# Kernel tuning notes

Hardware: AMD Instinct MI355X
Metric: run time of the kernel (lower is better)

Reference implementation:

```python
import math
import jax, jax.numpy as jnp
import numpy as np
from jax import lax

G_RATIO = 0.5       # g_ratio init arg
TMAX_RATIO = 0.25


def setup_inputs() -> dict:
    key = jax.random.key(0)
    k1, k2, k3, k4 = jax.random.split(key, 4)
    N = 4096
    cost_maps = jax.random.uniform(k1, (N,), jnp.float32)          # heuristic h(v)
    nodes = jax.random.uniform(k2, (N, 2), jnp.float32)            # coords (only size used)
    adj = (jax.random.uniform(k3, (N, N)) < 0.005).astype(jnp.float32)
    adj = jnp.maximum(adj, adj.T)                                  # symmetric PRM-like graph
    w = jax.random.uniform(k4, (N, N), jnp.float32, minval=0.1, maxval=1.0)
    weighted_adj = adj * w                                         # edge lengths
    return {"start_index": 0, "goal_index": N - 1, "cost_maps": cost_maps,
            "nodes": nodes, "adj": adj, "weighted_adj": weighted_adj}


def _astar_forward(start_index, goal_index, cost_maps, adj, weighted_adj):
    N = cost_maps.shape[0]
    inv_sqrt_n = 1.0 / math.sqrt(N)
    diag = jnp.arange(N)
    adj = adj.at[diag, diag].set(0.0)
    weighted_adj = jnp.where(jnp.isinf(weighted_adj), 0.0, weighted_adj)
    weighted_adj = weighted_adj.at[diag, diag].set(0.0)

    h = cost_maps
    goal_maps = jnp.zeros((N,), cost_maps.dtype).at[goal_index].set(1.0)
    open0 = jnp.zeros((N,), cost_maps.dtype).at[start_index].set(1.0)
    hist0 = jnp.zeros((N,), cost_maps.dtype)
    g0 = weighted_adj[start_index]
    parents0 = jnp.full((N,), float(goal_index), cost_maps.dtype)
    Tmax = int(TMAX_RATIO * N)  # training-mode budget

    def step(carry, t):
        open_m, hist, g, parents, done, t_final = carry
        f = G_RATIO * g + (1.0 - G_RATIO) * h
        f_exp = jnp.exp(-f * inv_sqrt_n) * open_m
        denom = jnp.sum(f_exp)
        y = f_exp / jnp.where(denom == 0.0, 1.0, denom)  # guard only hits after done
        ind = jnp.argmax(y)
        y_hard = jnp.zeros_like(y).at[ind].set(1.0)
        snm = lax.stop_gradient(y_hard - y) + y  # straight-through one-hot select
        solved = jnp.sum(snm * goal_maps) >= 1e-8
        open2 = jnp.clip(open_m - snm, 0.0, 1.0)
        hist2 = jnp.clip(hist + snm, 0.0, 1.0)
        neighbor = (snm @ adj) * (1.0 - open2) * (1.0 - hist2)   # row-gather via matvec
        g2 = g[ind] + weighted_adj[ind]                          # tentative g through ind
        idx = lax.stop_gradient(((1.0 - open2) * (1.0 - hist2) + open2 * (g > g2).astype(g.dtype)) * neighbor)
        g_new = lax.stop_gradient(g2 * idx + g * (1.0 - idx))
        open3 = lax.stop_gradient(jnp.clip(open2 + idx, 0.0, 1.0))
        parents_new = ind.astype(parents.dtype) * idx + parents * (1.0 - idx)
        keep = done  # freeze state after goal found (mimics torch break)
        carry_out = (jnp.where(keep, open_m, open3),
                     jnp.where(keep, hist, hist2),
                     jnp.where(keep, g, g_new),
                     jnp.where(keep, parents, parents_new),
                     done | solved,
                     jnp.where(keep, t_final, t))
        return carry_out, None

    init = (open0, hist0, g0, parents0, jnp.array(False), jnp.int32(0))
    (open_m, hist, g, parents, done, t_final), _ = lax.scan(
        step, init, jnp.arange(Tmax, dtype=jnp.int32))

    # backtrack: path_maps[loc]=1; loc=parents[loc], repeated t_final times
    parents_i = parents.astype(jnp.int32)
    path0 = goal_maps.astype(jnp.int32)
    loc0 = parents_i[goal_index]

    def bt(carry, i):
        path, loc = carry
        do = i < t_final
        path = jnp.where(do, path.at[loc].set(1), path)
        loc = jnp.where(do, parents_i[loc], loc)
        return (path, loc), None

    (path_maps, _), _ = lax.scan(bt, (path0, loc0), jnp.arange(Tmax, dtype=jnp.int32))
    return hist, path_maps


def reference(start_index, goal_index, cost_maps, nodes, adj, weighted_adj):
    # training-mode forward: returns (histories, path_maps)
    return _astar_forward(start_index, goal_index, cost_maps, adj, weighted_adj)
```

## Files before the change

### kernel.cpp

```cpp
#include <hip/hip_runtime.h>
#include <math.h>


#define NN    4096
#define TMAXI 1024
#define CAP   96
#define STR   96

__device__ __forceinline__ float fexp_of(float g, float h, float open) {
    float f = __fadd_rn(__fmul_rn(0.5f, g), __fmul_rn(0.5f, h));
    return __fmul_rn(expf(__fmul_rn(-f, 0.015625f)), open);
}

template <int CTRL, int RMASK>
__device__ __forceinline__ double dpp_mov_d(double x) {
    int lo = __double2loint(x), hi = __double2hiint(x);
    lo = __builtin_amdgcn_update_dpp(lo, lo, CTRL, RMASK, 0xf, false);
    hi = __builtin_amdgcn_update_dpp(hi, hi, CTRL, RMASK, 0xf, false);
    return __hiloint2double(hi, lo);
}

__device__ __forceinline__ double wave_max_f64(double x) {
    x = fmax(x, dpp_mov_d<0x111, 0xf>(x));
    x = fmax(x, dpp_mov_d<0x112, 0xf>(x));
    x = fmax(x, dpp_mov_d<0x114, 0xf>(x));
    x = fmax(x, dpp_mov_d<0x118, 0xf>(x));
    x = fmax(x, dpp_mov_d<0x142, 0xa>(x));
    x = fmax(x, dpp_mov_d<0x143, 0xc>(x));
    int lo = __builtin_amdgcn_readlane(__double2loint(x), 63);
    int hi = __builtin_amdgcn_readlane(__double2hiint(x), 63);
    return __hiloint2double(hi, lo);
}

__global__ __launch_bounds__(256)
void build_csr(const float* __restrict__ wadj, float2* __restrict__ ent)
{
    __shared__ int lcnt;
    const int r = blockIdx.x;
    if (threadIdx.x == 0) lcnt = 0;
    __syncthreads();
    const float4* wrow = (const float4*)(wadj + (size_t)r * NN);
    for (int c = 0; c < NN / (256 * 4); ++c) {
        int t4 = c * 256 + threadIdx.x;
        float4 w4 = wrow[t4];
        float wv[4] = {w4.x, w4.y, w4.z, w4.w};
        #pragma unroll
        for (int k = 0; k < 4; ++k) {
            int col = t4 * 4 + k;
            float w = wv[k];
            if (col != r && w != 0.0f && !isinf(w)) {
                int p = atomicAdd(&lcnt, 1);
                if (p < CAP)
                    ent[(size_t)r * STR + p] =
                        make_float2(__int_as_float(col), w);
            }
        }
    }
    __syncthreads();
    int base = min(lcnt, CAP);
    for (int p = base + (int)threadIdx.x; p < CAP; p += 256)
        ent[(size_t)r * STR + p] = make_float2(__int_as_float(r), 0.0f);
}

__global__ __launch_bounds__(128, 1)
void astar_fwd9(const int* __restrict__ start_p,
                const int* __restrict__ goal_p,
                const float* __restrict__ cost_maps,
                const float* __restrict__ wadj,
                const float2* __restrict__ ent,
                float* __restrict__ scratch,
                float* __restrict__ out)
{
    __shared__ __align__(16) unsigned long long ls_key[NN];
    __shared__ __align__(16) float2 ls_gp[NN];
    __shared__ __align__(16) float ls_h[NN];
    __shared__ __align__(16) unsigned long long ls_bm[64];

    const int tid = threadIdx.x;

    if (tid >= 64) {
        const float4* p = (const float4*)ent;
        const int total = NN * (STR / 2);
        float acc = 0.0f;
        int l = tid - 64;
        #pragma unroll 4
        for (int i = l; i < total; i += 64) acc += p[i].x;
        scratch[l] = acc;
        return;
    }

    const int lane  = tid;
    const int start = start_p[0];
    const int goal  = goal_p[0];

    {
        const float4* c4 = (const float4*)cost_maps;
        const float4* w4 = (const float4*)(wadj + (size_t)start * NN);
        const float gf = (float)goal;
        for (int c = 0; c < NN / (64 * 4); ++c) {
            int j4 = c * 64 + lane;
            float4 hv4 = c4[j4];
            float4 gv4 = w4[j4];
            if (start >= j4 * 4 && start < j4 * 4 + 4)
                ((float*)&gv4)[start - j4 * 4] = 0.0f;
            ((float4*)ls_h)[j4] = hv4;
            float gv[4] = {gv4.x, gv4.y, gv4.z, gv4.w};
            #pragma unroll
            for (int k = 0; k < 4; ++k)
                ls_gp[j4 * 4 + k] = make_float2(gv[k], gf);
        }
        for (int c = 0; c < (int)(NN * sizeof(unsigned long long) /
                                  (64 * sizeof(float4))); ++c)
            ((float4*)ls_key)[c * 64 + lane] = make_float4(0.f, 0.f, 0.f, 0.f);
        ls_bm[lane] = 0ull;
        if (lane == 0) {
            float fe = fexp_of(0.0f, ls_h[start], 1.0f);
            unsigned long long kb = 0x3FF0000000000000ull
                | ((unsigned long long)__float_as_uint(fe) << 12)
                | (unsigned)(4095 - start);
            ls_key[start] = kb;
            ls_bm[start >> 6] = kb;
        }
    }

    int ind = start;
    unsigned long long closedm = 0ull;
    int tf = 0;

    for (int t = 0; t < TMAXI; ++t) {
        const int b = ind >> 6;

        const float2* row = ent + (size_t)ind * STR;
        float2 e0 = row[lane];
        float2 e1 = make_float2(0.0f, 0.0f);
        if (lane < 32) e1 = row[64 + lane];
        double bm_v = __longlong_as_double((long long)ls_bm[lane]);
        double kb_v = __longlong_as_double(
                          (long long)ls_key[(b << 6) + lane]);
        float  gind = ls_gp[ind].x;

        double kx = kb_v;
        if (lane == (ind & 63)) kx = 0.0;
        if (kx <= 1.0) kx = 0.0;
        double K_b = wave_max_f64(kx);

        if (lane == 0) {
            ls_key[ind] = 0x3FF0000000000000ull;
            ls_bm[b] = (unsigned long long)__double_as_longlong(K_b);
        }
        if (lane == b) closedm |= (1ull << (ind & 63));

        const float indf = (float)ind;
        double nk0 = 0.0, nk1 = 0.0;

        {
            int j = __float_as_int(e0.x);
            unsigned long long kj = ls_key[j];
            float hj = ls_h[j];
            if (kj == 0ull) {
                float g2 = __fadd_rn(gind, e0.y);
                float fe = fexp_of(g2, hj, 1.0f);
                unsigned long long kb = 0x3FF0000000000000ull
                    | ((unsigned long long)__float_as_uint(fe) << 12)
                    | (unsigned)(4095 - j);
                ls_gp[j]  = make_float2(g2, indf);
                ls_key[j] = kb;
                atomicMax(&ls_bm[j >> 6], kb);
                nk0 = __longlong_as_double((long long)kb);
            }
        }
        if (lane < 32) {
            int j = __float_as_int(e1.x);
            unsigned long long kj = ls_key[j];
            float hj = ls_h[j];
            if (kj == 0ull) {
                float g2 = __fadd_rn(gind, e1.y);
                float fe = fexp_of(g2, hj, 1.0f);
                unsigned long long kb = 0x3FF0000000000000ull
                    | ((unsigned long long)__float_as_uint(fe) << 12)
                    | (unsigned)(4095 - j);
                ls_gp[j]  = make_float2(g2, indf);
                ls_key[j] = kb;
                atomicMax(&ls_bm[j >> 6], kb);
                nk1 = __longlong_as_double((long long)kb);
            }
        }

        tf = t;
        if (ind == goal) break;

        double bmx = (lane == b) ? 0.0 : bm_v;
        double loc = fmax(fmax(bmx, kx), fmax(nk0, nk1));
        double M1 = wave_max_f64(loc);
        int ind_next;
        if (M1 > 1.0) {
            unsigned long long mb = (unsigned long long)__double_as_longlong(M1);
            ind_next = 4095 - (int)(mb & 0xFFFu);
        } else {
            ind_next = 0;
        }
        ind = __builtin_amdgcn_readfirstlane(ind_next);
    }

    ls_bm[lane] = closedm;
    for (int c = 0; c < NN / (64 * 4); ++c)
        ((float4*)ls_h)[c * 64 + lane] = make_float4(0.f, 0.f, 0.f, 0.f);
    if (lane == 0) {
        ls_h[goal] = 1.0f;
        int loc = (int)ls_gp[goal].y;
        for (int i = 0; i < tf; ++i) {
            if (ls_h[loc] != 0.0f) break;
            ls_h[loc] = 1.0f;
            loc = (int)ls_gp[loc].y;
        }
    }
    for (int c = 0; c < NN / (64 * 4); ++c) {
        int j4 = c * 64 + lane;
        unsigned long long m = ls_bm[j4 >> 4];
        unsigned int bits = (unsigned int)(m >> ((j4 & 15) * 4)) & 0xFu;
        float4 hist4;
        hist4.x = (bits & 1u) ? 1.0f : 0.0f;
        hist4.y = (bits & 2u) ? 1.0f : 0.0f;
        hist4.z = (bits & 4u) ? 1.0f : 0.0f;
        hist4.w = (bits & 8u) ? 1.0f : 0.0f;
        ((float4*)out)[j4]        = hist4;
        ((float4*)(out + NN))[j4] = ((const float4*)ls_h)[j4];
    }
}

__device__ __forceinline__ float clip01(float x) {
    return fminf(fmaxf(x, 0.0f), 1.0f);
}

__global__ __launch_bounds__(1024, 1)
void astar_fwd(const int* __restrict__ start_p,
               const int* __restrict__ goal_p,
               const float* __restrict__ cost_maps,
               const float* __restrict__ adj,
               const float* __restrict__ wadj,
               float* __restrict__ out)
{
    __shared__ __align__(16) float ls_open[NN];
    __shared__ __align__(16) float ls_hist[NN];
    __shared__ __align__(16) float ls_g[NN];
    __shared__ __align__(16) float ls_par[NN];
    __shared__ __align__(16) float ls_fe[NN];
    __shared__ __align__(16) float ls_h[NN];
    __shared__ float red_v[16];
    __shared__ float red_s[16];
    __shared__ int   red_i[16];
    __shared__ float bc_snm, bc_gind;
    __shared__ int   bc_ind, ls_done, ls_tf;

    const int tid   = threadIdx.x;
    const int start = start_p[0];
    const int goal  = goal_p[0];

    for (int k = 0; k < 4; ++k) {
        int j = tid * 4 + k;
        float hv = cost_maps[j];
        float gv = wadj[(size_t)start * NN + j];
        if (j == start) gv = 0.0f;
        float ov = (j == start) ? 1.0f : 0.0f;
        ls_h[j] = hv; ls_g[j] = gv; ls_open[j] = ov;
        ls_hist[j] = 0.0f; ls_par[j] = (float)goal;
        ls_fe[j] = fexp_of(gv, hv, ov);
    }
    if (tid == 0) { ls_done = 0; ls_tf = 0; }
    __syncthreads();

    for (int t = 0; t < TMAXI; ++t) {
        float4 fe4 = *(const float4*)&ls_fe[tid * 4];
        float v0 = fe4.x, v1 = fe4.y, v2 = fe4.z, v3 = fe4.w;
        float sum = ((v0 + v1) + v2) + v3;
        float best = v0; int bi = tid * 4;
        if (v1 > best) { best = v1; bi = tid * 4 + 1; }
        if (v2 > best) { best = v2; bi = tid * 4 + 2; }
        if (v3 > best) { best = v3; bi = tid * 4 + 3; }
        #pragma unroll
        for (int off = 32; off > 0; off >>= 1) {
            float ov = __shfl_down(best, off);
            int   oi = __shfl_down(bi, off);
            float os = __shfl_down(sum, off);
            sum += os;
            if (ov > best || (ov == best && oi < bi)) { best = ov; bi = oi; }
        }
        if ((tid & 63) == 0) {
            int w = tid >> 6;
            red_v[w] = best; red_s[w] = sum; red_i[w] = bi;
        }
        __syncthreads();
        if (tid == 0) {
            float denom = red_s[0]; best = red_v[0]; bi = red_i[0];
            #pragma unroll
            for (int w = 1; w < 16; ++w) {
                denom += red_s[w];
                if (red_v[w] > best || (red_v[w] == best && red_i[w] < bi)) {
                    best = red_v[w]; bi = red_i[w];
                }
            }
            int ind = bi;
            float dg = (denom == 0.0f) ? 1.0f : denom;
            float y_ind = ls_fe[ind] / dg;
            float snm = __fadd_rn(__fsub_rn(1.0f, y_ind), y_ind);
            ls_open[ind] = clip01(__fsub_rn(ls_open[ind], snm));
            ls_hist[ind] = clip01(__fadd_rn(ls_hist[ind], snm));
            ls_fe[ind]   = fexp_of(ls_g[ind], ls_h[ind], ls_open[ind]);
            bc_ind = ind; bc_snm = snm; bc_gind = ls_g[ind];
            ls_tf = t;
            if (ind == goal && snm >= 1e-8f) ls_done = 1;
        }
        __syncthreads();
        {
            const int   ind  = bc_ind;
            const float snm  = bc_snm;
            const float gind = bc_gind;
            const float indf = (float)ind;
            float4 a4 = ((const float4*)(adj  + (size_t)ind * NN))[tid];
            float4 w4 = ((const float4*)(wadj + (size_t)ind * NN))[tid];
            float av[4] = {a4.x, a4.y, a4.z, a4.w};
            float wvv[4] = {w4.x, w4.y, w4.z, w4.w};
            #pragma unroll
            for (int k = 0; k < 4; ++k) {
                int j = tid * 4 + k;
                float a = av[k], w = wvv[k];
                if (j == ind) { a = 0.0f; w = 0.0f; }
                if (a != 0.0f) {
                    float o = ls_open[j], hi = ls_hist[j], gj = ls_g[j];
                    float one_o = __fsub_rn(1.0f, o);
                    float one_h = __fsub_rn(1.0f, hi);
                    float sm    = __fmul_rn(snm, a);
                    float neigh = __fmul_rn(__fmul_rn(sm, one_o), one_h);
                    float g2    = __fadd_rn(gind, w);
                    float cmp   = (gj > g2) ? 1.0f : 0.0f;
                    float s   = __fadd_rn(__fmul_rn(one_o, one_h),
                                          __fmul_rn(o, cmp));
                    float idx = __fmul_rn(s, neigh);
                    if (idx != 0.0f) {
                        float omi = __fsub_rn(1.0f, idx);
                        float gn = __fadd_rn(__fmul_rn(g2, idx),
                                             __fmul_rn(gj, omi));
                        float on = clip01(__fadd_rn(o, idx));
                        float pn = __fadd_rn(__fmul_rn(indf, idx),
                                             __fmul_rn(ls_par[j], omi));
                        ls_g[j] = gn; ls_open[j] = on; ls_par[j] = pn;
                        ls_fe[j] = fexp_of(gn, ls_h[j], on);
                    }
                }
            }
        }
        __syncthreads();
        if (ls_done) break;
    }

    for (int k = 0; k < 4; ++k) {
        int j = tid * 4 + k;
        out[j] = ls_hist[j];
        out[NN + j] = (j == goal) ? 1.0f : 0.0f;
    }
    __syncthreads();
    if (tid == 0) {
        int tfv = ls_tf;
        int loc = (int)ls_par[goal];
        for (int i = 0; i < tfv; ++i) {
            out[NN + loc] = 1.0f;
            loc = (int)ls_par[loc];
        }
    }
}

extern "C" void kernel_launch(void* const* d_in, const int* in_sizes, int n_in,
                              void* d_out, int out_size, void* d_ws, size_t ws_size,
                              hipStream_t stream)
{
    const int*   start_p = (const int*)d_in[0];
    const int*   goal_p  = (const int*)d_in[1];
    const float* cost    = (const float*)d_in[2];
    const float* adj     = (const float*)d_in[4];
    const float* wadj    = (const float*)d_in[5];
    float* out = (float*)d_out;

    const size_t csr_bytes = (size_t)NN * STR * sizeof(float2);
    const size_t need = csr_bytes + 64 * sizeof(float);
    if (ws_size >= need) {
        float2* ent     = (float2*)d_ws;
        float*  scratch = (float*)((char*)d_ws + csr_bytes);
        build_csr<<<dim3(NN), dim3(256), 0, stream>>>(wadj, ent);
        astar_fwd9<<<dim3(1), dim3(128), 0, stream>>>(start_p, goal_p, cost,
                                                      wadj, ent, scratch, out);
    } else {
        astar_fwd<<<dim3(1), dim3(1024), 0, stream>>>(start_p, goal_p, cost,
                                                      adj, wadj, out);
    }
}
```

Baseline: 557.4 us.

## Pack CSR rows as SoA with u16 columns and pre-gathered heuristic values

The CSR row layout becomes structure-of-arrays per row: 16-bit column indices, weights, and neighbour heuristic values gathered from cost_maps at build time. The serial A* loop then reads h directly from the row instead of through a dependent LDS lookup, and the exp/key arithmetic is computed before the visited check so it can overlap the LDS load latency. This shortens the per-iteration critical path of the single-wave loop. In exchange each row grows from 768 to 960 bytes, and the build kernel does extra scattered reads of cost.

Result: slower. 667.4 us (+19.7%).

```diff
diff --git a/kernel.cpp b/kernel.cpp
--- a/kernel.cpp
+++ b/kernel.cpp
@@ -5,7 +5,8 @@
 #define NN    4096
 #define TMAXI 1024
 #define CAP   96
-#define STR   96
+#define ROWB  960
+#define STR9  96
 
 __device__ __forceinline__ float fexp_of(float g, float h, float open) {
     float f = __fadd_rn(__fmul_rn(0.5f, g), __fmul_rn(0.5f, h));
@@ -33,7 +34,213 @@
 }
 
 __global__ __launch_bounds__(256)
-void build_csr(const float* __restrict__ wadj, float2* __restrict__ ent)
+void build_csr10(const float* __restrict__ wadj,
+                 const float* __restrict__ cost,
+                 char* __restrict__ csr)
+{
+    __shared__ int lcnt;
+    const int r = blockIdx.x;
+    if (threadIdx.x == 0) lcnt = 0;
+    __syncthreads();
+    unsigned short* cols = (unsigned short*)(csr + (size_t)r * ROWB);
+    float* wv = (float*)(csr + (size_t)r * ROWB + 192);
+    float* hv = (float*)(csr + (size_t)r * ROWB + 576);
+    const float4* wrow = (const float4*)(wadj + (size_t)r * NN);
+    for (int c = 0; c < NN / (256 * 4); ++c) {
+        int t4 = c * 256 + threadIdx.x;
+        float4 w4 = wrow[t4];
+        float wvv[4] = {w4.x, w4.y, w4.z, w4.w};
+        #pragma unroll
+        for (int k = 0; k < 4; ++k) {
+            int col = t4 * 4 + k;
+            float w = wvv[k];
+            if (col != r && w != 0.0f && !isinf(w)) {
+                int p = atomicAdd(&lcnt, 1);
+                if (p < CAP) {
+                    cols[p] = (unsigned short)col;
+                    wv[p]   = w;
+                    hv[p]   = cost[col];
+                }
+            }
+        }
+    }
+    __syncthreads();
+    int base = min(lcnt, CAP);
+    for (int p = base + (int)threadIdx.x; p < CAP; p += 256) {
+        cols[p] = (unsigned short)r; wv[p] = 0.0f; hv[p] = 0.0f;
+    }
+}
+
+__global__ __launch_bounds__(128, 1)
+void astar_fwd10(const int* __restrict__ start_p,
+                 const int* __restrict__ goal_p,
+                 const float* __restrict__ cost_maps,
+                 const float* __restrict__ wadj,
+                 const char* __restrict__ csr,
+                 float* __restrict__ scratch,
+                 float* __restrict__ out)
+{
+    __shared__ __align__(16) unsigned long long ls_key[NN];
+    __shared__ __align__(16) float2 ls_gp[NN];
+    __shared__ __align__(16) float ls_pm[NN];
+    __shared__ __align__(16) unsigned long long ls_bm[64];
+
+    const int tid = threadIdx.x;
+
+    if (tid >= 64) {
+        const float4* p = (const float4*)csr;
+        const int total = NN * (ROWB / 16);
+        float acc = 0.0f;
+        int l = tid - 64;
+        #pragma unroll 4
+        for (int i = l; i < total; i += 64) acc += p[i].x;
+        scratch[l] = acc;
+        return;
+    }
+
+    const int lane  = tid;
+    const int start = start_p[0];
+    const int goal  = goal_p[0];
+
+    {
+        const float4* w4 = (const float4*)(wadj + (size_t)start * NN);
+        const float gf = (float)goal;
+        for (int c = 0; c < NN / (64 * 4); ++c) {
+            int j4 = c * 64 + lane;
+            float4 gv4 = w4[j4];
+            if (start >= j4 * 4 && start < j4 * 4 + 4)
+                ((float*)&gv4)[start - j4 * 4] = 0.0f;
+            float gv[4] = {gv4.x, gv4.y, gv4.z, gv4.w};
+            #pragma unroll
+            for (int k = 0; k < 4; ++k)
+                ls_gp[j4 * 4 + k] = make_float2(gv[k], gf);
+        }
+        for (int c = 0; c < (int)(NN * sizeof(unsigned long long) /
+                                  (64 * sizeof(float4))); ++c)
+            ((float4*)ls_key)[c * 64 + lane] = make_float4(0.f, 0.f, 0.f, 0.f);
+        ls_bm[lane] = 0ull;
+        if (lane == 0) {
+            float hs = cost_maps[start];
+            float fe = fexp_of(0.0f, hs, 1.0f);
+            unsigned long long kb = 0x3FF0000000000000ull
+                | ((unsigned long long)__float_as_uint(fe) << 12)
+                | (unsigned)(4095 - start);
+            ls_key[start] = kb;
+            ls_bm[start >> 6] = kb;
+        }
+    }
+
+    int ind = start;
+    unsigned long long closedm = 0ull;
+    int tf = 0;
+
+    for (int t = 0; t < TMAXI; ++t) {
+        const int b = ind >> 6;
+
+        const char* rb = csr + (size_t)ind * ROWB;
+        int   c0 = *(const unsigned short*)(rb + 2 * lane);
+        float w0 = *(const float*)(rb + 192 + 4 * lane);
+        float h0 = *(const float*)(rb + 576 + 4 * lane);
+        int c1 = ind; float w1 = 0.0f, h1 = 0.0f;
+        if (lane < 32) {
+            c1 = *(const unsigned short*)(rb + 128 + 2 * lane);
+            w1 = *(const float*)(rb + 448 + 4 * lane);
+            h1 = *(const float*)(rb + 832 + 4 * lane);
+        }
+        double bm_v = __longlong_as_double((long long)ls_bm[lane]);
+        double kb_v = __longlong_as_double(
+                          (long long)ls_key[(b << 6) + lane]);
+        float  gind = ls_gp[ind].x;
+
+        double kx = kb_v;
+        if (lane == (ind & 63)) kx = 0.0;
+        if (kx <= 1.0) kx = 0.0;
+        double K_b = wave_max_f64(kx);
+
+        if (lane == 0) {
+            ls_key[ind] = 0x3FF0000000000000ull;
+            ls_bm[b] = (unsigned long long)__double_as_longlong(K_b);
+        }
+        if (lane == b) closedm |= (1ull << (ind & 63));
+
+        const float indf = (float)ind;
+        double nk0 = 0.0, nk1 = 0.0;
+
+        {
+            int j = c0;
+            unsigned long long kj = ls_key[j];
+            float g2 = __fadd_rn(gind, w0);
+            float fe = fexp_of(g2, h0, 1.0f);
+            unsigned long long kb = 0x3FF0000000000000ull
+                | ((unsigned long long)__float_as_uint(fe) << 12)
+                | (unsigned)(4095 - j);
+            if (kj == 0ull) {
+                ls_gp[j]  = make_float2(g2, indf);
+                ls_key[j] = kb;
+                atomicMax(&ls_bm[j >> 6], kb);
+                nk0 = __longlong_as_double((long long)kb);
+            }
+        }
+        if (lane < 32) {
+            int j = c1;
+            unsigned long long kj = ls_key[j];
+            float g2 = __fadd_rn(gind, w1);
+            float fe = fexp_of(g2, h1, 1.0f);
+            unsigned long long kb = 0x3FF0000000000000ull
+                | ((unsigned long long)__float_as_uint(fe) << 12)
+                | (unsigned)(4095 - j);
+            if (kj == 0ull) {
+                ls_gp[j]  = make_float2(g2, indf);
+                ls_key[j] = kb;
+                atomicMax(&ls_bm[j >> 6], kb);
+                nk1 = __longlong_as_double((long long)kb);
+            }
+        }
+
+        tf = t;
+        if (ind == goal) break;
+
+        double bmx = (lane == b) ? 0.0 : bm_v;
+        double loc = fmax(fmax(bmx, kx), fmax(nk0, nk1));
+        double M1 = wave_max_f64(loc);
+        int ind_next;
+        if (M1 > 1.0) {
+            unsigned long long mb = (unsigned long long)__double_as_longlong(M1);
+            ind_next = 4095 - (int)(mb & 0xFFFu);
+        } else {
+            ind_next = 0;
+        }
+        ind = __builtin_amdgcn_readfirstlane(ind_next);
+    }
+
+    ls_bm[lane] = closedm;
+    for (int c = 0; c < NN / (64 * 4); ++c)
+        ((float4*)ls_pm)[c * 64 + lane] = make_float4(0.f, 0.f, 0.f, 0.f);
+    if (lane == 0) {
+        ls_pm[goal] = 1.0f;
+        int loc = (int)ls_gp[goal].y;
+        for (int i = 0; i < tf; ++i) {
+            if (ls_pm[loc] != 0.0f) break;
+            ls_pm[loc] = 1.0f;
+            loc = (int)ls_gp[loc].y;
+        }
+    }
+    for (int c = 0; c < NN / (64 * 4); ++c) {
+        int j4 = c * 64 + lane;
+        unsigned long long m = ls_bm[j4 >> 4];
+        unsigned int bits = (unsigned int)(m >> ((j4 & 15) * 4)) & 0xFu;
+        float4 hist4;
+        hist4.x = (bits & 1u) ? 1.0f : 0.0f;
+        hist4.y = (bits & 2u) ? 1.0f : 0.0f;
+        hist4.z = (bits & 4u) ? 1.0f : 0.0f;
+        hist4.w = (bits & 8u) ? 1.0f : 0.0f;
+        ((float4*)out)[j4]        = hist4;
+        ((float4*)(out + NN))[j4] = ((const float4*)ls_pm)[j4];
+    }
+}
+
+__global__ __launch_bounds__(256)
+void build_csr9(const float* __restrict__ wadj, float2* __restrict__ ent)
 {
     __shared__ int lcnt;
     const int r = blockIdx.x;
@@ -51,7 +258,7 @@
             if (col != r && w != 0.0f && !isinf(w)) {
                 int p = atomicAdd(&lcnt, 1);
                 if (p < CAP)
-                    ent[(size_t)r * STR + p] =
+                    ent[(size_t)r * STR9 + p] =
                         make_float2(__int_as_float(col), w);
             }
         }
@@ -59,7 +266,7 @@
     __syncthreads();
     int base = min(lcnt, CAP);
     for (int p = base + (int)threadIdx.x; p < CAP; p += 256)
-        ent[(size_t)r * STR + p] = make_float2(__int_as_float(r), 0.0f);
+        ent[(size_t)r * STR9 + p] = make_float2(__int_as_float(r), 0.0f);
 }
 
 __global__ __launch_bounds__(128, 1)
@@ -77,10 +284,9 @@
     __shared__ __align__(16) unsigned long long ls_bm[64];
 
     const int tid = threadIdx.x;
-
     if (tid >= 64) {
         const float4* p = (const float4*)ent;
-        const int total = NN * (STR / 2);
+        const int total = NN * (STR9 / 2);
         float acc = 0.0f;
         int l = tid - 64;
         #pragma unroll 4
@@ -88,11 +294,9 @@
         scratch[l] = acc;
         return;
     }
-
     const int lane  = tid;
     const int start = start_p[0];
     const int goal  = goal_p[0];
-
     {
         const float4* c4 = (const float4*)cost_maps;
         const float4* w4 = (const float4*)(wadj + (size_t)start * NN);
@@ -122,37 +326,29 @@
             ls_bm[start >> 6] = kb;
         }
     }
-
     int ind = start;
     unsigned long long closedm = 0ull;
     int tf = 0;
-
     for (int t = 0; t < TMAXI; ++t) {
         const int b = ind >> 6;
-
-        const float2* row = ent + (size_t)ind * STR;
+        const float2* row = ent + (size_t)ind * STR9;
         float2 e0 = row[lane];
         float2 e1 = make_float2(0.0f, 0.0f);
         if (lane < 32) e1 = row[64 + lane];
         double bm_v = __longlong_as_double((long long)ls_bm[lane]);
-        double kb_v = __longlong_as_double(
-                          (long long)ls_key[(b << 6) + lane]);
+        double kb_v = __longlong_as_double((long long)ls_key[(b << 6) + lane]);
         float  gind = ls_gp[ind].x;
-
         double kx = kb_v;
         if (lane == (ind & 63)) kx = 0.0;
         if (kx <= 1.0) kx = 0.0;
         double K_b = wave_max_f64(kx);
-
         if (lane == 0) {
             ls_key[ind] = 0x3FF0000000000000ull;
             ls_bm[b] = (unsigned long long)__double_as_longlong(K_b);
         }
         if (lane == b) closedm |= (1ull << (ind & 63));
-
         const float indf = (float)ind;
         double nk0 = 0.0, nk1 = 0.0;
-
         {
             int j = __float_as_int(e0.x);
             unsigned long long kj = ls_key[j];
@@ -185,10 +381,8 @@
                 nk1 = __longlong_as_double((long long)kb);
             }
         }
-
         tf = t;
         if (ind == goal) break;
-
         double bmx = (lane == b) ? 0.0 : bm_v;
         double loc = fmax(fmax(bmx, kx), fmax(nk0, nk1));
         double M1 = wave_max_f64(loc);
@@ -196,12 +390,9 @@
         if (M1 > 1.0) {
             unsigned long long mb = (unsigned long long)__double_as_longlong(M1);
             ind_next = 4095 - (int)(mb & 0xFFFu);
-        } else {
-            ind_next = 0;
-        }
+        } else ind_next = 0;
         ind = __builtin_amdgcn_readfirstlane(ind_next);
     }
-
     ls_bm[lane] = closedm;
     for (int c = 0; c < NN / (64 * 4); ++c)
         ((float4*)ls_h)[c * 64 + lane] = make_float4(0.f, 0.f, 0.f, 0.f);
@@ -380,12 +571,18 @@
     const float* wadj    = (const float*)d_in[5];
     float* out = (float*)d_out;
 
-    const size_t csr_bytes = (size_t)NN * STR * sizeof(float2);
-    const size_t need = csr_bytes + 64 * sizeof(float);
-    if (ws_size >= need) {
+    const size_t csr10_bytes = (size_t)NN * ROWB;
+    const size_t csr9_bytes  = (size_t)NN * STR9 * sizeof(float2);
+    if (ws_size >= csr10_bytes + 64 * sizeof(float)) {
+        char*  c10     = (char*)d_ws;
+        float* scratch = (float*)(c10 + csr10_bytes);
+        build_csr10<<<dim3(NN), dim3(256), 0, stream>>>(wadj, cost, c10);
+        astar_fwd10<<<dim3(1), dim3(128), 0, stream>>>(start_p, goal_p, cost,
+                                                       wadj, c10, scratch, out);
+    } else if (ws_size >= csr9_bytes + 64 * sizeof(float)) {
         float2* ent     = (float2*)d_ws;
-        float*  scratch = (float*)((char*)d_ws + csr_bytes);
-        build_csr<<<dim3(NN), dim3(256), 0, stream>>>(wadj, ent);
+        float*  scratch = (float*)((char*)d_ws + csr9_bytes);
+        build_csr9<<<dim3(NN), dim3(256), 0, stream>>>(wadj, ent);
         astar_fwd9<<<dim3(1), dim3(128), 0, stream>>>(start_p, goal_p, cost,
                                                       wadj, ent, scratch, out);
     } else {
```

## Speculatively prefetch second-best candidate's CSR row to hide gather latency

Applied to the files above, without the earlier changes.

Each serial A* step now computes a second wave max to find the runner-up open node and issues the global load of that node's CSR neighbor row one iteration early. If the next selected node matches the speculated candidate, the prefetched row is used, taking the global-memory latency off the serial critical path. The cost is an extra wave reduction and an extra row load per step, and the speculation only pays off when the next pick equals the current runner-up.

Result: slower. 698.2 us (+25.3%).

```diff
diff --git a/kernel.cpp b/kernel.cpp
--- a/kernel.cpp
+++ b/kernel.cpp
@@ -5,7 +5,7 @@
 #define NN    4096
 #define TMAXI 1024
 #define CAP   96
-#define STR   96
+#define STR9  96
 
 __device__ __forceinline__ float fexp_of(float g, float h, float open) {
     float f = __fadd_rn(__fmul_rn(0.5f, g), __fmul_rn(0.5f, h));
@@ -33,7 +33,7 @@
 }
 
 __global__ __launch_bounds__(256)
-void build_csr(const float* __restrict__ wadj, float2* __restrict__ ent)
+void build_csr9(const float* __restrict__ wadj, float2* __restrict__ ent)
 {
     __shared__ int lcnt;
     const int r = blockIdx.x;
@@ -51,7 +51,7 @@
             if (col != r && w != 0.0f && !isinf(w)) {
                 int p = atomicAdd(&lcnt, 1);
                 if (p < CAP)
-                    ent[(size_t)r * STR + p] =
+                    ent[(size_t)r * STR9 + p] =
                         make_float2(__int_as_float(col), w);
             }
         }
@@ -59,17 +59,17 @@
     __syncthreads();
     int base = min(lcnt, CAP);
     for (int p = base + (int)threadIdx.x; p < CAP; p += 256)
-        ent[(size_t)r * STR + p] = make_float2(__int_as_float(r), 0.0f);
+        ent[(size_t)r * STR9 + p] = make_float2(__int_as_float(r), 0.0f);
 }
 
 __global__ __launch_bounds__(128, 1)
-void astar_fwd9(const int* __restrict__ start_p,
-                const int* __restrict__ goal_p,
-                const float* __restrict__ cost_maps,
-                const float* __restrict__ wadj,
-                const float2* __restrict__ ent,
-                float* __restrict__ scratch,
-                float* __restrict__ out)
+void astar_fwd11(const int* __restrict__ start_p,
+                 const int* __restrict__ goal_p,
+                 const float* __restrict__ cost_maps,
+                 const float* __restrict__ wadj,
+                 const float2* __restrict__ ent,
+                 float* __restrict__ scratch,
+                 float* __restrict__ out)
 {
     __shared__ __align__(16) unsigned long long ls_key[NN];
     __shared__ __align__(16) float2 ls_gp[NN];
@@ -80,7 +80,7 @@
 
     if (tid >= 64) {
         const float4* p = (const float4*)ent;
-        const int total = NN * (STR / 2);
+        const int total = NN * (STR9 / 2);
         float acc = 0.0f;
         int l = tid - 64;
         #pragma unroll 4
@@ -123,21 +123,38 @@
         }
     }
 
-    int ind = start;
+    int ind  = start;
+    int cand = -1;
+    int spec_id = -1;
+    float2 s_e0 = make_float2(0.f, 0.f);
+    float2 s_e1 = make_float2(0.f, 0.f);
     unsigned long long closedm = 0ull;
     int tf = 0;
 
     for (int t = 0; t < TMAXI; ++t) {
         const int b = ind >> 6;
 
-        const float2* row = ent + (size_t)ind * STR;
-        float2 e0 = row[lane];
-        float2 e1 = make_float2(0.0f, 0.0f);
-        if (lane < 32) e1 = row[64 + lane];
+        const float2* row = ent + (size_t)ind * STR9;
+        float2 t0 = row[lane];
+        float2 t1 = make_float2(0.0f, 0.0f);
+        if (lane < 32) t1 = row[64 + lane];
+
+        float2 n0 = make_float2(0.0f, 0.0f), n1 = make_float2(0.0f, 0.0f);
+        if (cand >= 0) {
+            const float2* rw = ent + (size_t)cand * STR9;
+            n0 = rw[lane];
+            if (lane < 32) n1 = rw[64 + lane];
+        }
+
         double bm_v = __longlong_as_double((long long)ls_bm[lane]);
         double kb_v = __longlong_as_double(
                           (long long)ls_key[(b << 6) + lane]);
         float  gind = ls_gp[ind].x;
+
+        float2 e0, e1;
+        if (ind == spec_id) { e0 = s_e0; e1 = s_e1; }
+        else                { e0 = t0;   e1 = t1;   }
+        s_e0 = n0; s_e1 = n1; spec_id = cand;
 
         double kx = kb_v;
         if (lane == (ind & 63)) kx = 0.0;
@@ -190,8 +207,12 @@
         if (ind == goal) break;
 
         double bmx = (lane == b) ? 0.0 : bm_v;
-        double loc = fmax(fmax(bmx, kx), fmax(nk0, nk1));
-        double M1 = wave_max_f64(loc);
+        double a0 = fmax(bmx, kx), b0 = fmin(bmx, kx);
+        double a1 = fmax(nk0, nk1), b1 = fmin(nk0, nk1);
+        double l1 = fmax(a0, a1);
+        double l2 = fmax(fmin(a0, a1), fmax(b0, b1));
+
+        double M1 = wave_max_f64(l1);
         int ind_next;
         if (M1 > 1.0) {
             unsigned long long mb = (unsigned long long)__double_as_longlong(M1);
@@ -200,6 +221,17 @@
             ind_next = 0;
         }
         ind = __builtin_amdgcn_readfirstlane(ind_next);
+
+        double c2 = (l1 == M1) ? l2 : l1;
+        double M2 = wave_max_f64(c2);
+        int cn;
+        if (M2 > 1.0) {
+            unsigned long long mb2 = (unsigned long long)__double_as_longlong(M2);
+            cn = 4095 - (int)(mb2 & 0xFFFu);
+        } else {
+            cn = -1;
+        }
+        cand = __builtin_amdgcn_readfirstlane(cn);
     }
 
     ls_bm[lane] = closedm;
@@ -380,14 +412,14 @@
     const float* wadj    = (const float*)d_in[5];
     float* out = (float*)d_out;
 
-    const size_t csr_bytes = (size_t)NN * STR * sizeof(float2);
+    const size_t csr_bytes = (size_t)NN * STR9 * sizeof(float2);
     const size_t need = csr_bytes + 64 * sizeof(float);
     if (ws_size >= need) {
         float2* ent     = (float2*)d_ws;
         float*  scratch = (float*)((char*)d_ws + csr_bytes);
-        build_csr<<<dim3(NN), dim3(256), 0, stream>>>(wadj, ent);
-        astar_fwd9<<<dim3(1), dim3(128), 0, stream>>>(start_p, goal_p, cost,
-                                                      wadj, ent, scratch, out);
+        build_csr9<<<dim3(NN), dim3(256), 0, stream>>>(wadj, ent);
+        astar_fwd11<<<dim3(1), dim3(128), 0, stream>>>(start_p, goal_p, cost,
+                                                       wadj, ent, scratch, out);
     } else {
         astar_fwd<<<dim3(1), dim3(1024), 0, stream>>>(start_p, goal_p, cost,
                                                       adj, wadj, out);
```
